# Kernel tuning notes

Measured on AMD Instinct MI355X. Metric: run time of the kernel, lower is better.

Reference implementation:

```python
import jax, jax.numpy as jnp
import numpy as np

B = 131072
D = 512


def setup_inputs() -> dict:
    key = jax.random.key(0)
    kx, kL, kb, kc = jax.random.split(key, 4)
    x = jax.random.normal(kx, (B, D), dtype=jnp.float32)
    L = jax.random.normal(kL, (D, D), dtype=jnp.float32)
    b = jax.random.normal(kb, (D,), dtype=jnp.float32)
    c = jax.random.normal(kc, (1,), dtype=jnp.float32)
    return {"x": x, "L": L, "b": b, "c": c}


def reference(x, L, b, c):
    # y = diag(x L L' x') + x b + c == sum((x @ L)**2, -1) + x @ b + c
    # Avoids the naive O(B^2 D) GEMM and O(B^2) intermediate.
    xL = x @ L                      # [B, D]
    quad = jnp.sum(xL * xL, axis=-1)  # [B]
    y = quad + x @ b + c            # [B] (c broadcasts from [1])
    return y[:, None]               # [B, 1]
```

## Files before the change

### kernel.cpp

```cpp
#include <hip/hip_runtime.h>
#include <stdint.h>

#define D_DIM   512
#define BM      64
#define THREADS 256
#define NBLOCKS 2048

typedef __attribute__((ext_vector_type(8))) __bf16 bf16x8;
typedef __attribute__((ext_vector_type(4))) float  f32x4;

__device__ __forceinline__ unsigned short f32_to_bf16_rne(float f) {
    uint32_t u = __builtin_bit_cast(uint32_t, f);
    u += 0x7FFFu + ((u >> 16) & 1u);
    return (unsigned short)(u >> 16);
}

__global__ void prep_lt(const float* __restrict__ L, unsigned short* __restrict__ Ltf) {
    int o = blockIdx.x * 256 + threadIdx.x;
    #pragma unroll
    for (int i = 0; i < 4; ++i) {
        int idx  = o + i * 65536;
        int e    = idx & 7;
        int l    = (idx >> 3) & 63;
        int tile = idx >> 9;
        int ntg  = tile & 31;
        int ks   = tile >> 5;
        int n    = ntg * 16 + (l & 15);
        int k    = ks * 32 + (l >> 4) * 8 + e;
        Ltf[idx] = f32_to_bf16_rne(L[k * 512 + n]);
    }
}

__global__ void prep_bt(const float* __restrict__ b, unsigned short* __restrict__ Btf) {
    int idx = blockIdx.x * 256 + threadIdx.x;
    int e  = idx & 7;
    int l  = (idx >> 3) & 63;
    int ks = idx >> 9;
    int ln = l & 15, g = l >> 4;
    float v = (ln == 0) ? b[ks * 32 + g * 8 + e] : 0.f;
    Btf[idx] = f32_to_bf16_rne(v);
}

__global__ __launch_bounds__(THREADS, 2)
void psd_main(const float* __restrict__ x, const unsigned short* __restrict__ Ltf,
              const unsigned short* __restrict__ Btf,
              const float* __restrict__ c, float* __restrict__ out) {
    __shared__ __align__(16) float As[2][BM * 128];
    __shared__ float wpart[4][BM];

    const int t    = threadIdx.x;
    const int w    = t >> 6;
    const int lane = t & 63;
    const int g    = lane >> 4;
    const int ln   = lane & 15;
    const int lo   = lane & 31;
    const int hi   = lane >> 5;

    char* AsB = (char*)&As[0][0];
    const char* xB = (const char*)x + (size_t)blockIdx.x * (BM * 2048);

    const unsigned short* LtW = Ltf + (size_t)w * 4096 + (size_t)lane * 8;
    const unsigned short* BtL = Btf + (size_t)lane * 8;

    f32x4 acc[4][8];
    f32x4 accb[4];
    #pragma unroll
    for (int m = 0; m < 4; ++m) {
        accb[m] = (f32x4){0.f, 0.f, 0.f, 0.f};
        #pragma unroll
        for (int nt = 0; nt < 8; ++nt) acc[m][nt] = (f32x4){0.f, 0.f, 0.f, 0.f};
    }

#define STAGE(Q)                                                                         \
    {                                                                                    \
        char* ldsw = AsB + ((Q) & 1) * 32768 + w * 8192;                                 \
        _Pragma("unroll")                                                                \
        for (int j = 0; j < 8; ++j) {                                                    \
            int rr = j * 2 + hi;                                           \
            const char* gsrc = xB + (size_t)(w * 16 + rr) * 2048 + (Q) * 512             \
                             + ((lo ^ rr) << 4);                                         \
            __builtin_amdgcn_global_load_lds(                                            \
                (const __attribute__((address_space(1))) void*)gsrc,                     \
                (__attribute__((address_space(3))) void*)(ldsw + j * 1024), 16, 0, 0);   \
        }                                                                                \
    }

#define COMPUTE(Q)                                                                       \
    {                                                                                    \
        const char* rb = AsB + ((Q) & 1) * 32768;                                        \
        _Pragma("unroll")                                                                \
        for (int kl = 0; kl < 4; ++kl) {                                                 \
            const int ks = (Q) * 4 + kl;                                                 \
            bf16x8 bfr[8];                                                               \
            _Pragma("unroll")                                                            \
            for (int nt = 0; nt < 8; ++nt)                                               \
                bfr[nt] = *(const bf16x8*)(LtW + (size_t)ks * 16384 + nt * 512);         \
            bf16x8 bt;                                                                   \
            if (w == 0) bt = *(const bf16x8*)(BtL + (size_t)ks * 512);                   \
            _Pragma("unroll")                                                            \
            for (int m = 0; m < 4; ++m) {                                                \
                const int row = m * 16 + ln;                                             \
                const int cb  = kl * 8 + g * 2;                                          \
                f32x4 f0 = *(const f32x4*)(rb + row * 512 + (((cb    ) ^ ln) << 4));     \
                f32x4 f1 = *(const f32x4*)(rb + row * 512 + (((cb + 1) ^ ln) << 4));     \
                bf16x8 a;                                                                \
                a[0] = (__bf16)f0[0]; a[1] = (__bf16)f0[1];                              \
                a[2] = (__bf16)f0[2]; a[3] = (__bf16)f0[3];                              \
                a[4] = (__bf16)f1[0]; a[5] = (__bf16)f1[1];                              \
                a[6] = (__bf16)f1[2]; a[7] = (__bf16)f1[3];                              \
                _Pragma("unroll")                                                        \
                for (int nt = 0; nt < 8; ++nt)                                           \
                    acc[m][nt] = __builtin_amdgcn_mfma_f32_16x16x32_bf16(a, bfr[nt], acc[m][nt], 0, 0, 0); \
                if (w == 0)                                                              \
                    accb[m] = __builtin_amdgcn_mfma_f32_16x16x32_bf16(a, bt, accb[m], 0, 0, 0); \
            }                                                                            \
        }                                                                                \
    }

    STAGE(0)
    __syncthreads();
    STAGE(1)
    COMPUTE(0)
    __syncthreads();
    STAGE(2)
    COMPUTE(1)
    __syncthreads();
    STAGE(3)
    COMPUTE(2)
    __syncthreads();
    COMPUTE(3)

#undef STAGE
#undef COMPUTE

    #pragma unroll
    for (int m = 0; m < 4; ++m) {
        #pragma unroll
        for (int r = 0; r < 4; ++r) {
            float s = 0.f;
            #pragma unroll
            for (int nt = 0; nt < 8; ++nt) { float vv = acc[m][nt][r]; s += vv * vv; }
            s += __shfl_xor(s, 1);
            s += __shfl_xor(s, 2);
            s += __shfl_xor(s, 4);
            s += __shfl_xor(s, 8);
            if (ln == 0) {
                if (w == 0) s += accb[m][r];
                wpart[w][m * 16 + g * 4 + r] = s;
            }
        }
    }
    __syncthreads();

    if (t < BM) {
        float y = c[0] + wpart[0][t] + wpart[1][t] + wpart[2][t] + wpart[3][t];
        out[(size_t)blockIdx.x * BM + t] = y;
    }
}

extern "C" void kernel_launch(void* const* d_in, const int* in_sizes, int n_in,
                              void* d_out, int out_size, void* d_ws, size_t ws_size,
                              hipStream_t stream) {
    const float* x = (const float*)d_in[0];
    const float* L = (const float*)d_in[1];
    const float* b = (const float*)d_in[2];
    const float* c = (const float*)d_in[3];
    float* out = (float*)d_out;
    unsigned short* Ltf = (unsigned short*)d_ws;
    unsigned short* Btf = Ltf + 262144;

    prep_lt<<<256, 256, 0, stream>>>(L, Ltf);
    prep_bt<<<32, 256, 0, stream>>>(b, Btf);
    psd_main<<<NBLOCKS, THREADS, 0, stream>>>(x, Ltf, Btf, c, out);
}
```

Before: 97.26 us.

## Split N across 8 waves and compute x·b in fp32 instead of MFMA

New measurement: 229.4 us. 136% more time.

```diff
diff --git a/kernel.cpp b/kernel.cpp
--- a/kernel.cpp
+++ b/kernel.cpp
@@ -3,7 +3,7 @@
 
 #define D_DIM   512
 #define BM      64
-#define THREADS 256
+#define THREADS 512
 #define NBLOCKS 2048
 
 typedef __attribute__((ext_vector_type(8))) __bf16 bf16x8;
@@ -31,22 +31,13 @@
     }
 }
 
-__global__ void prep_bt(const float* __restrict__ b, unsigned short* __restrict__ Btf) {
-    int idx = blockIdx.x * 256 + threadIdx.x;
-    int e  = idx & 7;
-    int l  = (idx >> 3) & 63;
-    int ks = idx >> 9;
-    int ln = l & 15, g = l >> 4;
-    float v = (ln == 0) ? b[ks * 32 + g * 8 + e] : 0.f;
-    Btf[idx] = f32_to_bf16_rne(v);
-}
-
-__global__ __launch_bounds__(THREADS, 2)
+__global__ __launch_bounds__(THREADS, 4)
 void psd_main(const float* __restrict__ x, const unsigned short* __restrict__ Ltf,
-              const unsigned short* __restrict__ Btf,
-              const float* __restrict__ c, float* __restrict__ out) {
+              const float* __restrict__ b, const float* __restrict__ c,
+              float* __restrict__ out) {
     __shared__ __align__(16) float As[2][BM * 128];
-    __shared__ float wpart[4][BM];
+    __shared__ float wpart[8][BM];
+    __shared__ float bpart[BM];
 
     const int t    = threadIdx.x;
     const int w    = t >> 6;
@@ -58,27 +49,26 @@
 
     char* AsB = (char*)&As[0][0];
     const char* xB = (const char*)x + (size_t)blockIdx.x * (BM * 2048);
+    const float4* b4 = (const float4*)b;
 
-    const unsigned short* LtW = Ltf + (size_t)w * 4096 + (size_t)lane * 8;
-    const unsigned short* BtL = Btf + (size_t)lane * 8;
+    const unsigned short* LtW = Ltf + (size_t)w * 2048 + (size_t)lane * 8;
 
-    f32x4 acc[4][8];
-    f32x4 accb[4];
+    f32x4 acc[4][4];
     #pragma unroll
-    for (int m = 0; m < 4; ++m) {
-        accb[m] = (f32x4){0.f, 0.f, 0.f, 0.f};
+    for (int m = 0; m < 4; ++m)
         #pragma unroll
-        for (int nt = 0; nt < 8; ++nt) acc[m][nt] = (f32x4){0.f, 0.f, 0.f, 0.f};
-    }
+        for (int nt = 0; nt < 4; ++nt)
+            acc[m][nt] = (f32x4){0.f, 0.f, 0.f, 0.f};
+    float bacc = 0.f;
 
 #define STAGE(Q)                                                                         \
     {                                                                                    \
-        char* ldsw = AsB + ((Q) & 1) * 32768 + w * 8192;                                 \
+        char* ldsw = AsB + ((Q) & 1) * 32768 + w * 4096;                                 \
         _Pragma("unroll")                                                                \
-        for (int j = 0; j < 8; ++j) {                                                    \
-            int rr = j * 2 + hi;                                           \
-            const char* gsrc = xB + (size_t)(w * 16 + rr) * 2048 + (Q) * 512             \
-                             + ((lo ^ rr) << 4);                                         \
+        for (int j = 0; j < 4; ++j) {                                                    \
+            const int row = w * 8 + j * 2 + hi;                                          \
+            const char* gsrc = xB + (size_t)row * 2048 + (Q) * 512                       \
+                             + ((lo ^ (row & 15)) << 4);                                 \
             __builtin_amdgcn_global_load_lds(                                            \
                 (const __attribute__((address_space(1))) void*)gsrc,                     \
                 (__attribute__((address_space(3))) void*)(ldsw + j * 1024), 16, 0, 0);   \
@@ -91,12 +81,10 @@
         _Pragma("unroll")                                                                \
         for (int kl = 0; kl < 4; ++kl) {                                                 \
             const int ks = (Q) * 4 + kl;                                                 \
-            bf16x8 bfr[8];                                                               \
+            bf16x8 bfr[4];                                                               \
             _Pragma("unroll")                                                            \
-            for (int nt = 0; nt < 8; ++nt)                                               \
+            for (int nt = 0; nt < 4; ++nt)                                               \
                 bfr[nt] = *(const bf16x8*)(LtW + (size_t)ks * 16384 + nt * 512);         \
-            bf16x8 bt;                                                                   \
-            if (w == 0) bt = *(const bf16x8*)(BtL + (size_t)ks * 512);                   \
             _Pragma("unroll")                                                            \
             for (int m = 0; m < 4; ++m) {                                                \
                 const int row = m * 16 + ln;                                             \
@@ -109,11 +97,25 @@
                 a[4] = (__bf16)f1[0]; a[5] = (__bf16)f1[1];                              \
                 a[6] = (__bf16)f1[2]; a[7] = (__bf16)f1[3];                              \
                 _Pragma("unroll")                                                        \
-                for (int nt = 0; nt < 8; ++nt)                                           \
+                for (int nt = 0; nt < 4; ++nt)                                           \
                     acc[m][nt] = __builtin_amdgcn_mfma_f32_16x16x32_bf16(a, bfr[nt], acc[m][nt], 0, 0, 0); \
-                if (w == 0)                                                              \
-                    accb[m] = __builtin_amdgcn_mfma_f32_16x16x32_bf16(a, bt, accb[m], 0, 0, 0); \
             }                                                                            \
+        }                                                                                \
+    }
+
+#define XB_PASS(Q)                                                                       \
+    {                                                                                    \
+        const char* rb = AsB + ((Q) & 1) * 32768;                                        \
+        const int r8  = lane & 7;                                                        \
+        const int cw  = lane >> 3;                                                       \
+        const int row = w * 8 + r8;                                                      \
+        const int rsw = row & 15;                                                        \
+        _Pragma("unroll")                                                                \
+        for (int i = 0; i < 4; ++i) {                                                    \
+            const int unit = cw * 4 + i;                                                 \
+            f32x4 xv = *(const f32x4*)(rb + row * 512 + ((unit ^ rsw) << 4));            \
+            float4 bv = b4[(Q) * 32 + unit];                                             \
+            bacc += xv[0] * bv.x + xv[1] * bv.y + xv[2] * bv.z + xv[3] * bv.w;           \
         }                                                                                \
     }
 
@@ -121,17 +123,22 @@
     __syncthreads();
     STAGE(1)
     COMPUTE(0)
+    XB_PASS(0)
     __syncthreads();
     STAGE(2)
     COMPUTE(1)
+    XB_PASS(1)
     __syncthreads();
     STAGE(3)
     COMPUTE(2)
+    XB_PASS(2)
     __syncthreads();
     COMPUTE(3)
+    XB_PASS(3)
 
 #undef STAGE
 #undef COMPUTE
+#undef XB_PASS
 
     #pragma unroll
     for (int m = 0; m < 4; ++m) {
@@ -139,21 +146,28 @@
         for (int r = 0; r < 4; ++r) {
             float s = 0.f;
             #pragma unroll
-            for (int nt = 0; nt < 8; ++nt) { float vv = acc[m][nt][r]; s += vv * vv; }
+            for (int nt = 0; nt < 4; ++nt) { float vv = acc[m][nt][r]; s += vv * vv; }
             s += __shfl_xor(s, 1);
             s += __shfl_xor(s, 2);
             s += __shfl_xor(s, 4);
             s += __shfl_xor(s, 8);
-            if (ln == 0) {
-                if (w == 0) s += accb[m][r];
-                wpart[w][m * 16 + g * 4 + r] = s;
-            }
+            if (ln == 0) wpart[w][m * 16 + g * 4 + r] = s;
         }
+    }
+
+    {
+        float s = bacc;
+        s += __shfl_xor(s, 8);
+        s += __shfl_xor(s, 16);
+        s += __shfl_xor(s, 32);
+        if (lane < 8) bpart[w * 8 + lane] = s;
     }
     __syncthreads();
 
     if (t < BM) {
-        float y = c[0] + wpart[0][t] + wpart[1][t] + wpart[2][t] + wpart[3][t];
+        float y = c[0] + bpart[t];
+        #pragma unroll
+        for (int ww = 0; ww < 8; ++ww) y += wpart[ww][t];
         out[(size_t)blockIdx.x * BM + t] = y;
     }
 }
@@ -167,9 +181,7 @@
     const float* c = (const float*)d_in[3];
     float* out = (float*)d_out;
     unsigned short* Ltf = (unsigned short*)d_ws;
-    unsigned short* Btf = Ltf + 262144;
 
     prep_lt<<<256, 256, 0, stream>>>(L, Ltf);
-    prep_bt<<<32, 256, 0, stream>>>(b, Btf);
-    psd_main<<<NBLOCKS, THREADS, 0, stream>>>(x, Ltf, Btf, c, out);
+    psd_main<<<NBLOCKS, THREADS, 0, stream>>>(x, Ltf, b, c, out);
 }
```
